# Optimization experiments

Measured on AMD Instinct MI355X. Metric: run time of the kernel, lower is better.

The kernel has to match this reference:

```python
import jax, jax.numpy as jnp
import numpy as np

ALPHA = 2000.0
TAU = 1e-07
K = 3
TOL = 1e-06
MAX_ITER = 50
T = 1048576  # 2**20
EPS = 1e-08


def setup_inputs() -> dict:
    key = jax.random.key(0)
    k1, k2 = jax.random.split(key)
    x = jax.random.normal(k1, (T,), dtype=jnp.float32)
    omega0 = jax.random.uniform(k2, (K,), dtype=jnp.float32)  # torch does 0.5*rand(K); scaled in reference
    return {"x": x, "omega0": omega0}


def _vmd(x, omega0):
    Tn = x.shape[0]
    freqs = jnp.arange(1, Tn + 1, dtype=jnp.float32) / Tn - 0.5 - 1.0 / Tn  # [T]
    f_hat = jnp.fft.fftshift(jnp.fft.fft(x.astype(jnp.complex64)))  # [T] complex64
    omega = 0.5 * omega0  # init == 1
    u0 = jnp.zeros((K, Tn), dtype=jnp.complex64)
    lam0 = jnp.zeros((Tn,), dtype=jnp.complex64)

    def step(carry, n):
        u_out, u_prev, lam_prev, om, done = carry
        # --- u_hat update (vectorized over k; torch k-loop uses stale omega) ---
        d_self = (freqs[None, :] - om[:, None]) ** 2            # [K,T]
        denom = d_self + TAU ** 2
        denom = denom.at[1:].add(d_self[:-1])                    # + (freqs - omega[k-1])^2 for k>0
        denom = denom.at[:-1].add(d_self[1:])                    # + (freqs - omega[k+1])^2 for k<K-1
        u_new = (f_hat[None, :] - lam_prev[None, :] / 2) / (1.0 + ALPHA * denom)  # [K,T]
        # --- omega update (DC == 0 branch) ---
        power = jnp.abs(u_new) ** 2                              # [K,T] float32
        om_new = jnp.sum(power * freqs[None, :], axis=1) / (jnp.sum(power, axis=1) + EPS)
        # --- dual ascent ---
        lam_new = lam_prev + TAU * (jnp.sum(u_new, axis=0) - f_hat)
        # --- convergence check every 10 outer iterations (torch break -> done flag) ---
        u_diff = jnp.sum(jnp.abs(u_new - u_prev) ** 2) / (jnp.sum(jnp.abs(u_prev) ** 2) + EPS)
        o_diff = jnp.sum(jnp.abs(om_new - jnp.roll(om_new, 1))) / K
        conv = (n % 10 == 0) & (u_diff < TOL) & (o_diff < TOL)
        new = (u_new, u_new, lam_new, om_new, done | conv)
        old = (u_out, u_prev, lam_prev, om, done)
        out = jax.tree_util.tree_map(lambda a, b: jnp.where(done, a, b), old, new)
        return out, None

    carry = (u0, u0, lam0, omega, jnp.array(False))
    (u_final, _, _, _, _), _ = jax.lax.scan(step, carry, jnp.arange(MAX_ITER))
    imfs = jnp.fft.ifft(jnp.fft.ifftshift(u_final, axes=1), axis=1).real.astype(x.dtype)  # [K,T]
    return imfs


def reference(x, omega0):
    return _vmd(x, omega0)
```

## Files before the change

kernel.cpp:

```cpp
#include <hip/hip_runtime.h>
#include <math.h>


#define TN        (1 << 20)
#define NBINS     1024
#define PPB       1024
#define FALPHA    2000.0f
#define FTAU      1e-7f
#define FTOL      1e-6f
#define FEPS      1e-8f
#define FTWO_PI   6.28318530717958647692f
#define FINV_T    (1.0f / 1048576.0f)

#define PADI(i)   ((i) + ((i) >> 4))
#define PBUF      1088

__device__ __forceinline__ float2 cmulf(float2 a, float2 b) {
    return make_float2(a.x * b.x - a.y * b.y, a.x * b.y + a.y * b.x);
}
__device__ __forceinline__ float2 cis_rev(float r, float sgn) {
    return make_float2(__builtin_amdgcn_cosf(r),
                       sgn * __builtin_amdgcn_sinf(r));
}
__device__ __forceinline__ float rlanef(float v, int l) {
    return __int_as_float(__builtin_amdgcn_readlane(__float_as_int(v), l));
}

__device__ __forceinline__ void g3f(float fr, float om0, float om1, float om2,
                                    float& g0, float& g1, float& g2) {
    const float tau2 = FTAU * FTAU;
    float d0 = fr - om0; d0 *= d0;
    float d1 = fr - om1; d1 *= d1;
    float d2 = fr - om2; d2 *= d2;
    g0 = __builtin_amdgcn_rcpf(1.0f + FALPHA * (d0 + d1 + tau2));
    g1 = __builtin_amdgcn_rcpf(1.0f + FALPHA * (d0 + d1 + d2 + tau2));
    g2 = __builtin_amdgcn_rcpf(1.0f + FALPHA * (d1 + d2 + tau2));
}

__device__ __forceinline__ float dpp_wave_sum(float x) {
    x += __int_as_float(__builtin_amdgcn_update_dpp(
             0, __float_as_int(x), 0x111, 0xf, 0xf, true));
    x += __int_as_float(__builtin_amdgcn_update_dpp(
             0, __float_as_int(x), 0x112, 0xf, 0xf, true));
    x += __int_as_float(__builtin_amdgcn_update_dpp(
             0, __float_as_int(x), 0x114, 0xf, 0xf, true));
    x += __int_as_float(__builtin_amdgcn_update_dpp(
             0, __float_as_int(x), 0x118, 0xf, 0xf, true));
    x += __int_as_float(__builtin_amdgcn_update_dpp(
             0, __float_as_int(x), 0x142, 0xf, 0xf, true));
    x += __int_as_float(__builtin_amdgcn_update_dpp(
             0, __float_as_int(x), 0x143, 0xf, 0xf, true));
    return x;
}
__device__ __forceinline__ float dpp_sum32(float x) {
    x += __int_as_float(__builtin_amdgcn_update_dpp(
             0, __float_as_int(x), 0x111, 0xf, 0xf, true));
    x += __int_as_float(__builtin_amdgcn_update_dpp(
             0, __float_as_int(x), 0x112, 0xf, 0xf, true));
    x += __int_as_float(__builtin_amdgcn_update_dpp(
             0, __float_as_int(x), 0x114, 0xf, 0xf, true));
    x += __int_as_float(__builtin_amdgcn_update_dpp(
             0, __float_as_int(x), 0x118, 0xf, 0xf, true));
    x += __int_as_float(__builtin_amdgcn_update_dpp(
             0, __float_as_int(x), 0x142, 0xf, 0xf, true));
    return x;
}

__global__ __launch_bounds__(256)
void k_binpart(const float2* __restrict__ in, float* __restrict__ pB,
               float* __restrict__ pM) {
    __shared__ float tile[32][33];
    const int bx = blockIdx.x * 32, by = blockIdx.y * 32;
    const int tx = threadIdx.x, ty = threadIdx.y;
#pragma unroll
    for (int j = 0; j < 32; j += 8) {
        const float2 v = in[(size_t)(by + ty + j) * 1024 + bx + tx];
        tile[ty + j][tx] = v.x * v.x + v.y * v.y;
    }
    __syncthreads();
    const int sIdx = blockIdx.y;
    const float d = ((float)(by + tx) - 511.5f) * FINV_T;
    const int lane = (tx + 32 * ty) & 63;
#pragma unroll
    for (int j = 0; j < 32; j += 8) {
        float s = tile[tx][ty + j];
        float m = s * d;
        s = dpp_sum32(s);
        m = dpp_sum32(m);
        if (lane == 31 || lane == 63) {
            const int bin = bx + ty + j;
            pB[bin * 32 + sIdx] = s;
            pM[bin * 32 + sIdx] = m;
        }
    }
}

__global__ __launch_bounds__(256)
void k_omega(const float* __restrict__ pB, const float* __restrict__ pM,
             const float* __restrict__ omega0,
             float* __restrict__ oomf, float* __restrict__ sgsb) {
    const int tid = threadIdx.x;
    const int lane = tid & 63, wid = tid >> 6;
    const float kA = -4.0f * FALPHA;

    float B[4], M[4], C[4], SG[4], gp[4];
    const float4* __restrict__ pB4 = (const float4*)pB;
    const float4* __restrict__ pM4 = (const float4*)pM;
#pragma unroll
    for (int i = 0; i < 4; ++i) {
        const int j = tid + 256 * i;
        float sb = 0.f, sm = 0.f;
#pragma unroll
        for (int s = 0; s < 8; ++s) {
            const float4 b = pB4[j * 8 + s];
            sb += b.x; sb += b.y; sb += b.z; sb += b.w;
            const float4 m = pM4[j * 8 + s];
            sm += m.x; sm += m.y; sm += m.z; sm += m.w;
        }
        B[i] = sb; M[i] = sm;
        C[i] = ((float)(j * PPB) + 511.5f) * FINV_T - 0.5f;
        SG[i] = 0.f; gp[i] = 0.f;
    }

    float om0 = 0.5f * omega0[0];
    float om1 = 0.5f * omega0[1];
    float om2 = 0.5f * omega0[2];
    float op0 = om0, op1 = om1, op2 = om2;
    float n0 = om0, n1 = om1, n2 = om2;
    float stop = 0.f;

    __shared__ float wsum[2][4][8];
    bool fin = true;

    for (int n = 0; n < 49; ++n) {
        if (n > 0) {
            if (stop != 0.f) { fin = false; break; }
            op0 = om0; op1 = om1; op2 = om2;
            om0 = n0; om1 = n1; om2 = n2;
#pragma unroll
            for (int i = 0; i < 4; ++i) SG[i] += gp[i] - 1.0f;
        }
        const int check = (n > 0 && n % 10 == 0);

        float a[8];
#pragma unroll
        for (int v = 0; v < 8; ++v) a[v] = 0.f;

#pragma unroll
        for (int i = 0; i < 4; ++i) {
            const float c  = C[i];
            const float Bv = B[i];
            const float M1 = M[i];
            const float e0 = c - om0, e1 = c - om1, e2 = c - om2;
            float g0, g1, g2;
            g3f(c, om0, om1, om2, g0, g1, g2);
            const float gsq0 = g0 * g0, gsq1 = g1 * g1, gsq2 = g2 * g2;
            const float gc0 = gsq0 * g0, gc1 = gsq1 * g1, gc2 = gsq2 * g2;
            const float Dp0 = e0 + e1, Dp1 = e0 + e1 + e2, Dp2 = e1 + e2;
            const float P0 = gsq0 * Bv + kA * Dp0 * gc0 * M1;
            const float P1 = gsq1 * Bv + kA * Dp1 * gc1 * M1;
            const float P2 = gsq2 * Bv + kA * Dp2 * gc2 * M1;
            a[0] += P0; a[1] += P1; a[2] += P2;
            a[3] += c * P0 + gsq0 * M1;
            a[4] += c * P1 + gsq1 * M1;
            a[5] += c * P2 + gsq2 * M1;
            gp[i] = g0 + g1 + g2;
            if (check) {
                float h0, h1, h2;
                g3f(c, op0, op1, op2, h0, h1, h2);
                const float d0 = g0 - h0, d1 = g1 - h1, d2 = g2 - h2;
                a[6] += Bv * (d0 * d0 + d1 * d1 + d2 * d2);
                a[7] += Bv * (h0 * h0 + h1 * h1 + h2 * h2);
            }
        }
#pragma unroll
        for (int v = 0; v < 6; ++v) a[v] = dpp_wave_sum(a[v]);
        if (check) {
            a[6] = dpp_wave_sum(a[6]);
            a[7] = dpp_wave_sum(a[7]);
        }
        if (lane == 63) {
            *(float4*)&wsum[n & 1][wid][0] = make_float4(a[0], a[1], a[2], a[3]);
            *(float4*)&wsum[n & 1][wid][4] = make_float4(a[4], a[5], a[6], a[7]);
        }
        __syncthreads();
        float r = 0.f;
#pragma unroll
        for (int w = 0; w < 4; ++w) r += wsum[n & 1][w][lane & 7];
        const float S0 = rlanef(r, 0), S1 = rlanef(r, 1), S2 = rlanef(r, 2);
        const float S3 = rlanef(r, 3), S4 = rlanef(r, 4), S5 = rlanef(r, 5);
        n0 = S3 * __builtin_amdgcn_rcpf(S0 + FEPS);
        n1 = S4 * __builtin_amdgcn_rcpf(S1 + FEPS);
        n2 = S5 * __builtin_amdgcn_rcpf(S2 + FEPS);
        if (check) {
            const float S6 = rlanef(r, 6), S7 = rlanef(r, 7);
            const float ud = S6 * __builtin_amdgcn_rcpf(S7 + FEPS);
            const float od = (fabsf(n0 - n2) + fabsf(n1 - n0) +
                              fabsf(n2 - n1)) * (1.0f / 3.0f);
            stop = (ud < FTOL && od < FTOL) ? 1.f : 0.f;
        }
    }

    if (fin) {
#pragma unroll
        for (int i = 0; i < 4; ++i) SG[i] += gp[i] - 1.0f;
        om0 = n0; om1 = n1; om2 = n2;
    }
#pragma unroll
    for (int i = 0; i < 4; ++i) sgsb[tid + 256 * i] = SG[i];
    if (tid == 0) { oomf[0] = om0; oomf[1] = om1; oomf[2] = om2; }
}

__device__ __forceinline__ float2* fft1024_stages(float2* bufA, float2* bufB,
                                                  int t, float dir) {
    float2* src = bufA;
    float2* dst = bufB;
    int Ns = 1;
#pragma unroll
    for (int s = 0; s < 5; ++s) {
        const int jm = t & (Ns - 1);
        float2 v0 = src[PADI(t)],       v1 = src[PADI(t + 256)];
        float2 v2 = src[PADI(t + 512)], v3 = src[PADI(t + 768)];
        const float rv = (float)jm * (0.25f / (float)Ns);
        float2 w1 = cis_rev(rv, dir);
        float2 w2 = cmulf(w1, w1);
        float2 w3 = cmulf(w2, w1);
        v1 = cmulf(v1, w1); v2 = cmulf(v2, w2); v3 = cmulf(v3, w3);
        float2 s0 = make_float2(v0.x + v2.x, v0.y + v2.y);
        float2 s1 = make_float2(v0.x - v2.x, v0.y - v2.y);
        float2 s2 = make_float2(v1.x + v3.x, v1.y + v3.y);
        float2 s3 = make_float2(v1.x - v3.x, v1.y - v3.y);
        float2 s3i = make_float2(-dir * s3.y, dir * s3.x);
        const int base = ((t - jm) << 2) + jm;
        dst[PADI(base)]          = make_float2(s0.x + s2.x, s0.y + s2.y);
        dst[PADI(base + Ns)]     = make_float2(s1.x + s3i.x, s1.y + s3i.y);
        dst[PADI(base + 2 * Ns)] = make_float2(s0.x - s2.x, s0.y - s2.y);
        dst[PADI(base + 3 * Ns)] = make_float2(s1.x - s3i.x, s1.y - s3i.y);
        __syncthreads();
        float2* tmp = src; src = dst; dst = tmp;
        Ns <<= 2;
    }
    return src;
}

__device__ __forceinline__ float2* fft1024_stages4(float2* bufA, float2* bufB,
                                                   int t, float dir) {
    float2* src = bufA;
    float2* dst = bufB;
    int Ns = 1;
#pragma unroll
    for (int s = 0; s < 5; ++s) {
        const int jm = t & (Ns - 1);
        const float rv = (float)jm * (0.25f / (float)Ns);
        float2 w1 = cis_rev(rv, dir);
        float2 w2 = cmulf(w1, w1);
        float2 w3 = cmulf(w2, w1);
        const int base = ((t - jm) << 2) + jm;
#pragma unroll
        for (int q = 0; q < 4; ++q) {
            const int o = q * PBUF;
            float2 v0 = src[o + PADI(t)],       v1 = src[o + PADI(t + 256)];
            float2 v2 = src[o + PADI(t + 512)], v3 = src[o + PADI(t + 768)];
            v1 = cmulf(v1, w1); v2 = cmulf(v2, w2); v3 = cmulf(v3, w3);
            float2 s0 = make_float2(v0.x + v2.x, v0.y + v2.y);
            float2 s1 = make_float2(v0.x - v2.x, v0.y - v2.y);
            float2 s2 = make_float2(v1.x + v3.x, v1.y + v3.y);
            float2 s3 = make_float2(v1.x - v3.x, v1.y - v3.y);
            float2 s3i = make_float2(-dir * s3.y, dir * s3.x);
            dst[o + PADI(base)]          = make_float2(s0.x + s2.x, s0.y + s2.y);
            dst[o + PADI(base + Ns)]     = make_float2(s1.x + s3i.x, s1.y + s3i.y);
            dst[o + PADI(base + 2 * Ns)] = make_float2(s0.x - s2.x, s0.y - s2.y);
            dst[o + PADI(base + 3 * Ns)] = make_float2(s1.x - s3i.x, s1.y - s3i.y);
        }
        __syncthreads();
        float2* tmp = src; src = dst; dst = tmp;
        Ns <<= 2;
    }
    return src;
}

__global__ __launch_bounds__(256)
void k_fft1024(const float2* __restrict__ in, float2* __restrict__ out,
               float dir) {
    __shared__ float2 bufA[PBUF];
    __shared__ float2 bufB[PBUF];
    const int row  = blockIdx.x;
    const float2* __restrict__ rin  = in  + (size_t)row * 1024;
    float2* __restrict__ rout = out + (size_t)row * 1024;
    const int t = threadIdx.x;
#pragma unroll
    for (int r = 0; r < 4; ++r) {
        const int c = t + 256 * r;
        bufA[PADI(c)] = rin[c];
    }
    __syncthreads();
    float2* src = fft1024_stages(bufA, bufB, t, dir);
#pragma unroll
    for (int r = 0; r < 4; ++r) {
        const int c = t + 256 * r;
        rout[c] = src[PADI(c)];
    }
}

__global__ __launch_bounds__(256)
void k_fftfwd_slab(const float* __restrict__ x, float2* __restrict__ sA) {
    __shared__ float2 bufA[4][PBUF];
    __shared__ float2 bufB[4][PBUF];
    const int a0 = blockIdx.x * 4;
    const int t  = threadIdx.x;
#pragma unroll
    for (int r = 0; r < 4; ++r) {
        const int p = t + 256 * r;
        const float4 v = *(const float4*)(x + (size_t)p * 1024 + a0);
        const int pi = PADI(p);
        bufA[0][pi] = make_float2( v.x, 0.f);
        bufA[1][pi] = make_float2(-v.y, 0.f);
        bufA[2][pi] = make_float2( v.z, 0.f);
        bufA[3][pi] = make_float2(-v.w, 0.f);
    }
    __syncthreads();
    float2* src = fft1024_stages4(&bufA[0][0], &bufB[0][0], t, -1.0f);
#pragma unroll
    for (int r = 0; r < 4; ++r) {
        const int c = t + 256 * r;
        const int ci = PADI(c);
        float2 o[4];
#pragma unroll
        for (int q = 0; q < 4; ++q) {
            const unsigned p = ((unsigned)(a0 + q) * (unsigned)c) & 1048575u;
            o[q] = cmulf(src[q * PBUF + ci], cis_rev((float)p * FINV_T, -1.0f));
        }
        float2* w = sA + (size_t)c * 1024 + a0;
        *(float4*)(w)     = make_float4(o[0].x, o[0].y, o[1].x, o[1].y);
        *(float4*)(w + 2) = make_float4(o[2].x, o[2].y, o[3].x, o[3].y);
    }
}

__global__ __launch_bounds__(256)
void k_ifft_slab(const float2* __restrict__ zin, float* __restrict__ out,
                 int zbase) {
    __shared__ float2 bufA[4][PBUF];
    __shared__ float2 bufB[4][PBUF];
    const int m0 = blockIdx.x * 4;
    const int zi = blockIdx.y;
    const int z  = zi + zbase;
    const int t  = threadIdx.x;
    const float2* __restrict__ Z = zin + (size_t)zi * TN;
#pragma unroll
    for (int r = 0; r < 4; ++r) {
        const int k = t + 256 * r;
        const float4 u0 = *(const float4*)(Z + (size_t)k * 1024 + m0);
        const float4 u1 = *(const float4*)(Z + (size_t)k * 1024 + m0 + 2);
        const int ki = PADI(k);
        bufA[0][ki] = make_float2(u0.x, u0.y);
        bufA[1][ki] = make_float2(u0.z, u0.w);
        bufA[2][ki] = make_float2(u1.x, u1.y);
        bufA[3][ki] = make_float2(u1.z, u1.w);
    }
    __syncthreads();
    float2* src = fft1024_stages4(&bufA[0][0], &bufB[0][0], t, 1.0f);
#pragma unroll
    for (int r = 0; r < 4; ++r) {
        const int m2 = t + 256 * r;
        const int mi = PADI(m2);
        float re[4], im[4];
#pragma unroll
        for (int q = 0; q < 4; ++q) {
            const float sgn = (q & 1) ? -FINV_T : FINV_T;
            const float2 v = src[q * PBUF + mi];
            re[q] = v.x * sgn;
            im[q] = v.y * sgn;
        }
        const size_t idx = (size_t)m2 * 1024 + m0;
        if (z == 0) {
            *(float4*)(out + idx) =
                make_float4(re[0], re[1], re[2], re[3]);
            *(float4*)(out + (size_t)TN + idx) =
                make_float4(im[0], im[1], im[2], im[3]);
        } else {
            *(float4*)(out + 2 * (size_t)TN + idx) =
                make_float4(re[0], re[1], re[2], re[3]);
        }
    }
}

__global__ __launch_bounds__(256)
void k_fftu(const float2* __restrict__ fhat, const float* __restrict__ sgsb,
            const float* __restrict__ oomf,
            float2* __restrict__ out, int zbase) {
    __shared__ float2 bufA[PBUF];
    __shared__ float2 bufB[PBUF];
    const int row = blockIdx.x & 1023;
    const int zi  = blockIdx.x >> 10;
    const int z   = zi + zbase;
    const float om0 = oomf[0], om1 = oomf[1], om2 = oomf[2];
    const float2* __restrict__ frow = fhat + (size_t)row * 1024;
    const int t = threadIdx.x;
#pragma unroll
    for (int r = 0; r < 4; ++r) {
        const int c = t + 256 * r;
        const float2 f = frow[c];
        const int tt = (c << 10) | row;
        const float fr = (float)tt * FINV_T - 0.5f;
        const float sc = 1.0f - 0.5f * FTAU * sgsb[tt >> 10];
        float g0, g1, g2;
        g3f(fr, om0, om1, om2, g0, g1, g2);
        const int tm = (TN - tt) & (TN - 1);
        const float frm = (float)tm * FINV_T - 0.5f;
        const float scm = 1.0f - 0.5f * FTAU * sgsb[tm >> 10];
        float h0, h1, h2;
        g3f(frm, om0, om1, om2, h0, h1, h2);
        float A, Bi;
        if (z == 0) {
            A  = 0.5f * (g0 * sc + h0 * scm);
            Bi = 0.5f * (g1 * sc + h1 * scm);
        } else {
            A  = 0.5f * (g2 * sc + h2 * scm);
            Bi = 0.f;
        }
        bufA[PADI(c)] = cmulf(f, make_float2(A, Bi));
    }
    __syncthreads();
    float2* src = fft1024_stages(bufA, bufB, t, 1.0f);
    float2* __restrict__ rout = out + (size_t)zi * TN + (size_t)row * 1024;
#pragma unroll
    for (int r = 0; r < 4; ++r) {
        const int c = t + 256 * r;
        const unsigned p = ((unsigned)row * (unsigned)c) & 1048575u;
        rout[c] = cmulf(src[PADI(c)], cis_rev((float)p * FINV_T, 1.0f));
    }
}

__global__ __launch_bounds__(256)
void k_fftu2(const float2* __restrict__ fhat, const float* __restrict__ sgsb,
             const float* __restrict__ oomf, float2* __restrict__ out) {
    __shared__ float2 bufA[PBUF];
    __shared__ float2 bufB[PBUF];
    const int row = blockIdx.x;
    const float om0 = oomf[0], om1 = oomf[1], om2 = oomf[2];
    const float2* __restrict__ frow = fhat + (size_t)row * 1024;
    const int t = threadIdx.x;
    float2 fsave[4];
    float  A2s[4];
    float2 tws[4];
#pragma unroll
    for (int r = 0; r < 4; ++r) {
        const int c = t + 256 * r;
        const float2 f = frow[c];
        const int tt = (c << 10) | row;
        const float fr = (float)tt * FINV_T - 0.5f;
        const float sc = 1.0f - 0.5f * FTAU * sgsb[tt >> 10];
        float g0, g1, g2;
        g3f(fr, om0, om1, om2, g0, g1, g2);
        const int tm = (TN - tt) & (TN - 1);
        const float frm = (float)tm * FINV_T - 0.5f;
        const float scm = 1.0f - 0.5f * FTAU * sgsb[tm >> 10];
        float h0, h1, h2;
        g3f(frm, om0, om1, om2, h0, h1, h2);
        const float A  = 0.5f * (g0 * sc + h0 * scm);
        const float Bi = 0.5f * (g1 * sc + h1 * scm);
        A2s[r]   = 0.5f * (g2 * sc + h2 * scm);
        fsave[r] = f;
        bufA[PADI(c)] = cmulf(f, make_float2(A, Bi));
    }
    __syncthreads();
    float2* src = fft1024_stages(bufA, bufB, t, 1.0f);
    float2* __restrict__ r0 = out + (size_t)row * 1024;
#pragma unroll
    for (int r = 0; r < 4; ++r) {
        const int c = t + 256 * r;
        const unsigned p = ((unsigned)row * (unsigned)c) & 1048575u;
        tws[r] = cis_rev((float)p * FINV_T, 1.0f);
        r0[c] = cmulf(src[PADI(c)], tws[r]);
    }
#pragma unroll
    for (int r = 0; r < 4; ++r) {
        const int c = t + 256 * r;
        bufA[PADI(c)] = cmulf(fsave[r], make_float2(A2s[r], 0.f));
    }
    __syncthreads();
    src = fft1024_stages(bufA, bufB, t, 1.0f);
    float2* __restrict__ r1 = out + (size_t)TN + (size_t)row * 1024;
#pragma unroll
    for (int r = 0; r < 4; ++r) {
        const int c = t + 256 * r;
        r1[c] = cmulf(src[PADI(c)], tws[r]);
    }
}

extern "C" void kernel_launch(void* const* d_in, const int* in_sizes, int n_in,
                              void* d_out, int out_size, void* d_ws, size_t ws_size,
                              hipStream_t stream) {
    (void)in_sizes; (void)n_in; (void)out_size;
    const float* x      = (const float*)d_in[0];
    const float* omega0 = (const float*)d_in[1];
    float* outp = (float*)d_out;
    char* ws = (char*)d_ws;

    const size_t MB = (size_t)1 << 20;
    const size_t KB = (size_t)1 << 10;
    float2* fhat = (float2*)(ws);
    float*  pB   = (float*)(ws + 8 * MB);
    float*  pM   = (float*)(ws + 8 * MB + 128 * KB);
    float*  sgsb = (float*)(ws + 8 * MB + 256 * KB);
    float*  oomf = (float*)(ws + 8 * MB + 264 * KB);
    const bool batch2 = ws_size >= 42 * MB;
    float2* sA = (float2*)(ws + 9 * MB);
    float2* sB = batch2 ? (float2*)(ws + 25 * MB)
                        : (float2*)(ws + 17 * MB);

    k_fftfwd_slab<<<256, 256, 0, stream>>>(x, sA);
    k_fft1024<<<1024, 256, 0, stream>>>(sA, fhat, -1.0f);

    k_binpart<<<dim3(32, 32), dim3(32, 8), 0, stream>>>(fhat, pB, pM);

    k_omega<<<1, 256, 0, stream>>>(pB, pM, omega0, oomf, sgsb);

    if (batch2) {
        k_fftu2<<<1024, 256, 0, stream>>>(fhat, sgsb, oomf, sB);
        k_ifft_slab<<<dim3(256, 2), 256, 0, stream>>>(sB, outp, 0);
    } else {
        for (int z = 0; z < 2; ++z) {
            k_fftu<<<1024, 256, 0, stream>>>(fhat, sgsb, oomf, sB, z);
            k_ifft_slab<<<dim3(256, 1), 256, 0, stream>>>(sB, outp, z);
        }
    }
}
```

Before: 165.8 us.

## Use 512-thread blocks so FFT slab and fused u-kernels split work across halves

The slab forward and inverse FFT kernels now launch 512 threads, and each half of the block transforms two of the four columns instead of one thread doing all four. The fused u-update kernel runs its two 1024-point FFTs concurrently in separate shared buffers, one per half-block, rather than one after the other. The aim is more parallelism per block, fewer serial FFT passes and lower register pressure, giving better latency hiding. The cost is larger blocks and more shared memory in k_fftu2, which can reduce occupancy.

Result: no change. 164.8 us (-0.6%).

```diff
diff --git a/kernel.cpp b/kernel.cpp
--- a/kernel.cpp
+++ b/kernel.cpp
@@ -243,8 +243,8 @@
     return src;
 }
 
-__device__ __forceinline__ float2* fft1024_stages4(float2* bufA, float2* bufB,
-                                                   int t, float dir) {
+__device__ __forceinline__ float2* fft1024_stages2x(float2* bufA, float2* bufB,
+                                                    int t, int h, float dir) {
     float2* src = bufA;
     float2* dst = bufB;
     int Ns = 1;
@@ -257,8 +257,8 @@
         float2 w3 = cmulf(w2, w1);
         const int base = ((t - jm) << 2) + jm;
 #pragma unroll
-        for (int q = 0; q < 4; ++q) {
-            const int o = q * PBUF;
+        for (int qq = 0; qq < 2; ++qq) {
+            const int o = (2 * h + qq) * PBUF;
             float2 v0 = src[o + PADI(t)],       v1 = src[o + PADI(t + 256)];
             float2 v2 = src[o + PADI(t + 512)], v3 = src[o + PADI(t + 768)];
             v1 = cmulf(v1, w1); v2 = cmulf(v2, w2); v3 = cmulf(v3, w3);
@@ -302,15 +302,16 @@
     }
 }
 
-__global__ __launch_bounds__(256)
+__global__ __launch_bounds__(512)
 void k_fftfwd_slab(const float* __restrict__ x, float2* __restrict__ sA) {
     __shared__ float2 bufA[4][PBUF];
     __shared__ float2 bufB[4][PBUF];
-    const int a0 = blockIdx.x * 4;
-    const int t  = threadIdx.x;
-#pragma unroll
-    for (int r = 0; r < 4; ++r) {
-        const int p = t + 256 * r;
+    const int a0  = blockIdx.x * 4;
+    const int tid = threadIdx.x;
+    const int t = tid & 255, h = tid >> 8;
+#pragma unroll
+    for (int r = 0; r < 2; ++r) {
+        const int p = tid + 512 * r;
         const float4 v = *(const float4*)(x + (size_t)p * 1024 + a0);
         const int pi = PADI(p);
         bufA[0][pi] = make_float2( v.x, 0.f);
@@ -319,10 +320,10 @@
         bufA[3][pi] = make_float2(-v.w, 0.f);
     }
     __syncthreads();
-    float2* src = fft1024_stages4(&bufA[0][0], &bufB[0][0], t, -1.0f);
-#pragma unroll
-    for (int r = 0; r < 4; ++r) {
-        const int c = t + 256 * r;
+    float2* src = fft1024_stages2x(&bufA[0][0], &bufB[0][0], t, h, -1.0f);
+#pragma unroll
+    for (int r = 0; r < 2; ++r) {
+        const int c = tid + 512 * r;
         const int ci = PADI(c);
         float2 o[4];
 #pragma unroll
@@ -336,19 +337,20 @@
     }
 }
 
-__global__ __launch_bounds__(256)
+__global__ __launch_bounds__(512)
 void k_ifft_slab(const float2* __restrict__ zin, float* __restrict__ out,
                  int zbase) {
     __shared__ float2 bufA[4][PBUF];
     __shared__ float2 bufB[4][PBUF];
-    const int m0 = blockIdx.x * 4;
-    const int zi = blockIdx.y;
-    const int z  = zi + zbase;
-    const int t  = threadIdx.x;
+    const int m0  = blockIdx.x * 4;
+    const int zi  = blockIdx.y;
+    const int z   = zi + zbase;
+    const int tid = threadIdx.x;
+    const int t = tid & 255, h = tid >> 8;
     const float2* __restrict__ Z = zin + (size_t)zi * TN;
 #pragma unroll
-    for (int r = 0; r < 4; ++r) {
-        const int k = t + 256 * r;
+    for (int r = 0; r < 2; ++r) {
+        const int k = tid + 512 * r;
         const float4 u0 = *(const float4*)(Z + (size_t)k * 1024 + m0);
         const float4 u1 = *(const float4*)(Z + (size_t)k * 1024 + m0 + 2);
         const int ki = PADI(k);
@@ -358,10 +360,10 @@
         bufA[3][ki] = make_float2(u1.z, u1.w);
     }
     __syncthreads();
-    float2* src = fft1024_stages4(&bufA[0][0], &bufB[0][0], t, 1.0f);
-#pragma unroll
-    for (int r = 0; r < 4; ++r) {
-        const int m2 = t + 256 * r;
+    float2* src = fft1024_stages2x(&bufA[0][0], &bufB[0][0], t, h, 1.0f);
+#pragma unroll
+    for (int r = 0; r < 2; ++r) {
+        const int m2 = tid + 512 * r;
         const int mi = PADI(m2);
         float re[4], im[4];
 #pragma unroll
@@ -431,21 +433,19 @@
     }
 }
 
-__global__ __launch_bounds__(256)
+__global__ __launch_bounds__(512)
 void k_fftu2(const float2* __restrict__ fhat, const float* __restrict__ sgsb,
              const float* __restrict__ oomf, float2* __restrict__ out) {
-    __shared__ float2 bufA[PBUF];
-    __shared__ float2 bufB[PBUF];
+    __shared__ float2 b0A[PBUF], b0B[PBUF];
+    __shared__ float2 b1A[PBUF], b1B[PBUF];
     const int row = blockIdx.x;
     const float om0 = oomf[0], om1 = oomf[1], om2 = oomf[2];
     const float2* __restrict__ frow = fhat + (size_t)row * 1024;
-    const int t = threadIdx.x;
-    float2 fsave[4];
-    float  A2s[4];
-    float2 tws[4];
-#pragma unroll
-    for (int r = 0; r < 4; ++r) {
-        const int c = t + 256 * r;
+    const int tid = threadIdx.x;
+    const int t = tid & 255, h = tid >> 8;
+#pragma unroll
+    for (int e = 0; e < 2; ++e) {
+        const int c = tid + 512 * e;
         const float2 f = frow[c];
         const int tt = (c << 10) | row;
         const float fr = (float)tt * FINV_T - 0.5f;
@@ -459,32 +459,21 @@
         g3f(frm, om0, om1, om2, h0, h1, h2);
         const float A  = 0.5f * (g0 * sc + h0 * scm);
         const float Bi = 0.5f * (g1 * sc + h1 * scm);
-        A2s[r]   = 0.5f * (g2 * sc + h2 * scm);
-        fsave[r] = f;
-        bufA[PADI(c)] = cmulf(f, make_float2(A, Bi));
+        const float A2 = 0.5f * (g2 * sc + h2 * scm);
+        const int ci = PADI(c);
+        b0A[ci] = cmulf(f, make_float2(A, Bi));
+        b1A[ci] = make_float2(f.x * A2, f.y * A2);
     }
     __syncthreads();
+    float2* bufA = h ? b1A : b0A;
+    float2* bufB = h ? b1B : b0B;
     float2* src = fft1024_stages(bufA, bufB, t, 1.0f);
-    float2* __restrict__ r0 = out + (size_t)row * 1024;
+    float2* __restrict__ rout = out + (size_t)h * TN + (size_t)row * 1024;
 #pragma unroll
     for (int r = 0; r < 4; ++r) {
         const int c = t + 256 * r;
         const unsigned p = ((unsigned)row * (unsigned)c) & 1048575u;
-        tws[r] = cis_rev((float)p * FINV_T, 1.0f);
-        r0[c] = cmulf(src[PADI(c)], tws[r]);
-    }
-#pragma unroll
-    for (int r = 0; r < 4; ++r) {
-        const int c = t + 256 * r;
-        bufA[PADI(c)] = cmulf(fsave[r], make_float2(A2s[r], 0.f));
-    }
-    __syncthreads();
-    src = fft1024_stages(bufA, bufB, t, 1.0f);
-    float2* __restrict__ r1 = out + (size_t)TN + (size_t)row * 1024;
-#pragma unroll
-    for (int r = 0; r < 4; ++r) {
-        const int c = t + 256 * r;
-        r1[c] = cmulf(src[PADI(c)], tws[r]);
+        rout[c] = cmulf(src[PADI(c)], cis_rev((float)p * FINV_T, 1.0f));
     }
 }
 
@@ -509,7 +498,7 @@
     float2* sB = batch2 ? (float2*)(ws + 25 * MB)
                         : (float2*)(ws + 17 * MB);
 
-    k_fftfwd_slab<<<256, 256, 0, stream>>>(x, sA);
+    k_fftfwd_slab<<<256, 512, 0, stream>>>(x, sA);
     k_fft1024<<<1024, 256, 0, stream>>>(sA, fhat, -1.0f);
 
     k_binpart<<<dim3(32, 32), dim3(32, 8), 0, stream>>>(fhat, pB, pM);
@@ -517,12 +506,12 @@
     k_omega<<<1, 256, 0, stream>>>(pB, pM, omega0, oomf, sgsb);
 
     if (batch2) {
-        k_fftu2<<<1024, 256, 0, stream>>>(fhat, sgsb, oomf, sB);
-        k_ifft_slab<<<dim3(256, 2), 256, 0, stream>>>(sB, outp, 0);
+        k_fftu2<<<1024, 512, 0, stream>>>(fhat, sgsb, oomf, sB);
+        k_ifft_slab<<<dim3(256, 2), 512, 0, stream>>>(sB, outp, 0);
     } else {
         for (int z = 0; z < 2; ++z) {
             k_fftu<<<1024, 256, 0, stream>>>(fhat, sgsb, oomf, sB, z);
-            k_ifft_slab<<<dim3(256, 1), 256, 0, stream>>>(sB, outp, z);
-        }
-    }
-}
+            k_ifft_slab<<<dim3(256, 1), 512, 0, stream>>>(sB, outp, z);
+        }
+    }
+}
```
